# Optimization experiments

Measured on AMD Instinct MI355X. Metric: run time of the kernel, lower is better.

Reference implementation:

```python
import jax, jax.numpy as jnp
import numpy as np

N = 16384
E = 524288
IN_DIM = 128
LATENT = 48
EPS = 1e-5


def setup_inputs() -> dict:
    key = jax.random.key(0)
    ks = jax.random.split(key, 20)
    def rn(k, shape, scale=0.05):
        return jax.random.normal(k, shape, dtype=jnp.float32) * scale
    return {
        "x": jax.random.normal(ks[0], (N, IN_DIM), dtype=jnp.float32),
        "edge_index": jax.random.randint(ks[1], (2, E), 0, N, dtype=jnp.int64),
        "W1": rn(ks[2], (IN_DIM, 256)), "b1": jnp.zeros((256,), jnp.float32),
        "W2": rn(ks[3], (256, 128)),    "b2": jnp.zeros((128,), jnp.float32),
        "W3": rn(ks[4], (128, LATENT)), "b3": jnp.zeros((LATENT,), jnp.float32),
        "skip_W": rn(ks[5], (IN_DIM, LATENT)), "skip_b": jnp.zeros((LATENT,), jnp.float32),
        "bn_gamma": jnp.ones((256,), jnp.float32), "bn_beta": jnp.zeros((256,), jnp.float32),
        "bn_mean": rn(ks[6], (256,), 0.01), "bn_var": jnp.ones((256,), jnp.float32),
        "dpW1": rn(ks[7], (LATENT, 64)), "dpb1": jnp.zeros((64,), jnp.float32),
        "dpW2": rn(ks[8], (64, 1)),      "dpb2": jnp.zeros((1,), jnp.float32),
    }


def _gcn_norm(edge_index, n):
    # add self-loops, compute symmetric normalization (PyG gcn_norm)
    loops = jnp.arange(n, dtype=edge_index.dtype)
    src = jnp.concatenate([edge_index[0], loops])
    dst = jnp.concatenate([edge_index[1], loops])
    deg = jax.ops.segment_sum(jnp.ones_like(dst, dtype=jnp.float32), dst, num_segments=n)
    dinv = jnp.where(deg > 0, jax.lax.rsqrt(jnp.maximum(deg, 1.0)), 0.0)
    norm = dinv[src] * dinv[dst]  # [E+N]
    return src, dst, norm


def _gcn_conv(x, src, dst, norm, W, b, n):
    h = x @ W                                    # [N, out]
    msg = h[src] * norm[:, None]                 # gather + scale, [E+N, out]
    return jax.ops.segment_sum(msg, dst, num_segments=n) + b


def reference(x, edge_index, W1, b1, W2, b2, W3, b3, skip_W, skip_b,
              bn_gamma, bn_beta, bn_mean, bn_var, dpW1, dpb1, dpW2, dpb2):
    n = x.shape[0]
    src, dst, norm = _gcn_norm(edge_index, n)
    identity = x @ skip_W + skip_b
    h = _gcn_conv(x, src, dst, norm, W1, b1, n)
    # BatchNorm1d (inference mode: running stats), then ReLU; dropout = identity (eval)
    h = (h - bn_mean) * jax.lax.rsqrt(bn_var + EPS) * bn_gamma + bn_beta
    h = jax.nn.relu(h)
    h = jax.nn.relu(_gcn_conv(h, src, dst, norm, W2, b2, n))
    z = _gcn_conv(h, src, dst, norm, W3, b3, n) + identity   # [N, latent]
    adj_recon = jax.nn.sigmoid(z @ z.T)                      # [N, N]
    degree_pred = (jax.nn.relu(z @ dpW1 + dpb1) @ dpW2 + dpb2).squeeze(-1)
    return z, adj_recon, degree_pred
```

## Files before the change

### kernel.cpp

```cpp
#include <hip/hip_runtime.h>
#include <hip/hip_bf16.h>
#include <math.h>

#define NN   16384
#define EE   524288
#define TOTE (EE + NN)

typedef short s16x8 __attribute__((ext_vector_type(8)));
typedef float f32x16 __attribute__((ext_vector_type(16)));

__device__ inline unsigned short bf16r(float f) {
    unsigned int u = __float_as_uint(f);
    return (unsigned short)((u + 0x7FFFu + ((u >> 16) & 1u)) >> 16);
}

__global__ void k_prep(const float* __restrict__ x,  const float* __restrict__ W1,
                       const float* __restrict__ W2, const float* __restrict__ W3,
                       const float* __restrict__ skW,
                       unsigned short* __restrict__ xb,  unsigned short* __restrict__ W1t,
                       unsigned short* __restrict__ W2t, unsigned short* __restrict__ W3t,
                       unsigned short* __restrict__ skWt,
                       int* __restrict__ deg, int* __restrict__ cur) {
    const int S0 = NN * 128;
    const int S1 = S0 + 256 * 128;
    const int S2 = S1 + 128 * 256;
    const int S3 = S2 + 64 * 128;
    const int S4 = S3 + 64 * 128;
    int i = blockIdx.x * 256 + threadIdx.x;
    if (i < NN) { deg[i] = 0; cur[i] = 0; }
    if (i < S0) { xb[i] = bf16r(x[i]); }
    else if (i < S1) { int j = i - S0; int n = j >> 7, k = j & 127; W1t[j] = bf16r(W1[k * 256 + n]); }
    else if (i < S2) { int j = i - S1; int n = j >> 8, k = j & 255; W2t[j] = bf16r(W2[k * 128 + n]); }
    else if (i < S3) { int j = i - S2; int n = j >> 7, k = j & 127; W3t[j] = (n < 48) ? bf16r(W3[k * 48 + n]) : 0; }
    else if (i < S4) { int j = i - S3; int n = j >> 7, k = j & 127; skWt[j] = (n < 48) ? bf16r(skW[k * 48 + n]) : 0; }
}

__global__ void k_deg(const int* __restrict__ ei, int* __restrict__ deg) {
    int e = blockIdx.x * blockDim.x + threadIdx.x;
    if (e < EE) atomicAdd(&deg[ei[EE + e]], 1);
}

__global__ __launch_bounds__(1024) void k_scan(const int* __restrict__ deg,
                                               int* __restrict__ off,
                                               float* __restrict__ dinv) {
    __shared__ int part[1024];
    int t = threadIdx.x;
    int base = t * 16;
    int loc[16];
    int s = 0;
#pragma unroll
    for (int q = 0; q < 16; q++) {
        loc[q] = deg[base + q] + 1;
        dinv[base + q] = rsqrtf((float)loc[q]);
        s += loc[q];
    }
    part[t] = s;
    __syncthreads();
    for (int d = 1; d < 1024; d <<= 1) {
        int v = (t >= d) ? part[t - d] : 0;
        __syncthreads();
        part[t] += v;
        __syncthreads();
    }
    int ex = (t == 0) ? 0 : part[t - 1];
#pragma unroll
    for (int q = 0; q < 16; q++) { off[base + q] = ex; ex += loc[q]; }
    if (t == 1023) off[NN] = ex;
}

__global__ void k_fill(const int* __restrict__ ei, const int* __restrict__ off,
                       int* __restrict__ cur, const float* __restrict__ dinv,
                       int* __restrict__ cs, float* __restrict__ cw) {
    int e = blockIdx.x * blockDim.x + threadIdx.x;
    if (e >= TOTE) return;
    int s, d;
    if (e < EE) { s = ei[e]; d = ei[EE + e]; }
    else        { s = d = e - EE; }
    int pos = off[d] + atomicAdd(&cur[d], 1);
    cs[pos] = s;
    cw[pos] = dinv[s] * dinv[d];
}

__global__ void k_bnfold(const float* __restrict__ b1, const float* __restrict__ gamma,
                         const float* __restrict__ beta, const float* __restrict__ mean,
                         const float* __restrict__ var,
                         float* __restrict__ A, float* __restrict__ C) {
    int j = threadIdx.x;
    float a = gamma[j] * rsqrtf(var[j] + 1e-5f);
    A[j] = a;
    C[j] = (b1[j] - mean[j]) * a + beta[j];
}

template <int MODE>
__global__ void k_agg128(const unsigned short* __restrict__ H, const int* __restrict__ off,
                         const int* __restrict__ cs, const float* __restrict__ cw,
                         const float* __restrict__ bias, unsigned short* __restrict__ Y) {
    int node = blockIdx.x * 4 + (threadIdx.x >> 6);
    int lane = threadIdx.x & 63;
    int s0 = off[node], cnt = off[node + 1] - s0;
    const unsigned int* Hp = (const unsigned int*)H;
    float ax = 0.f, ay = 0.f;
    for (int base = 0; base < cnt; base += 64) {
        int nb = cnt - base; if (nb > 64) nb = 64;
        int vi = 0; float vw = 0.f;
        if (lane < nb) { vi = cs[s0 + base + lane]; vw = cw[s0 + base + lane]; }
        int e = 0;
        for (; e + 4 <= nb; e += 4) {
            int   i0 = __shfl(vi, e + 0), i1 = __shfl(vi, e + 1);
            int   i2 = __shfl(vi, e + 2), i3 = __shfl(vi, e + 3);
            float w0 = __shfl(vw, e + 0), w1 = __shfl(vw, e + 1);
            float w2 = __shfl(vw, e + 2), w3 = __shfl(vw, e + 3);
            unsigned int u0 = Hp[(size_t)i0 * 64 + lane];
            unsigned int u1 = Hp[(size_t)i1 * 64 + lane];
            unsigned int u2 = Hp[(size_t)i2 * 64 + lane];
            unsigned int u3 = Hp[(size_t)i3 * 64 + lane];
            ax += __uint_as_float(u0 << 16) * w0 + __uint_as_float(u1 << 16) * w1
                + __uint_as_float(u2 << 16) * w2 + __uint_as_float(u3 << 16) * w3;
            ay += __uint_as_float(u0 & 0xffff0000u) * w0 + __uint_as_float(u1 & 0xffff0000u) * w1
                + __uint_as_float(u2 & 0xffff0000u) * w2 + __uint_as_float(u3 & 0xffff0000u) * w3;
        }
        for (; e < nb; e++) {
            int i0 = __shfl(vi, e); float w0 = __shfl(vw, e);
            unsigned int u0 = Hp[(size_t)i0 * 64 + lane];
            ax += __uint_as_float(u0 << 16) * w0;
            ay += __uint_as_float(u0 & 0xffff0000u) * w0;
        }
    }
    if constexpr (MODE == 2) {
        ax = fmaxf(ax + bias[2 * lane], 0.f);
        ay = fmaxf(ay + bias[2 * lane + 1], 0.f);
    }
    unsigned int o = ((unsigned int)bf16r(ay) << 16) | bf16r(ax);
    ((unsigned int*)Y)[(size_t)node * 64 + lane] = o;
}

__global__ void k_aggz(const float* __restrict__ H, const int* __restrict__ off,
                       const int* __restrict__ cs, const float* __restrict__ cw,
                       const float* __restrict__ b3, const float* __restrict__ idb,
                       const float* __restrict__ dpW1, const float* __restrict__ dpb1,
                       const float* __restrict__ dpW2, const float* __restrict__ dpb2,
                       float* __restrict__ zout, unsigned short* __restrict__ zb,
                       float* __restrict__ dpout) {
    int node = blockIdx.x * 4 + (threadIdx.x >> 6);
    int lane = threadIdx.x & 63;
    int s0 = off[node], cnt = off[node + 1] - s0;
    float a = 0.f;
    for (int base = 0; base < cnt; base += 64) {
        int nb = cnt - base; if (nb > 64) nb = 64;
        int vi = 0; float vw = 0.f;
        if (lane < nb) { vi = cs[s0 + base + lane]; vw = cw[s0 + base + lane]; }
        int e = 0;
        for (; e + 4 <= nb; e += 4) {
            int   i0 = __shfl(vi, e + 0), i1 = __shfl(vi, e + 1);
            int   i2 = __shfl(vi, e + 2), i3 = __shfl(vi, e + 3);
            float w0 = __shfl(vw, e + 0), w1 = __shfl(vw, e + 1);
            float w2 = __shfl(vw, e + 2), w3 = __shfl(vw, e + 3);
            if (lane < 48) {
                float v0 = H[(size_t)i0 * 64 + lane];
                float v1 = H[(size_t)i1 * 64 + lane];
                float v2 = H[(size_t)i2 * 64 + lane];
                float v3 = H[(size_t)i3 * 64 + lane];
                a += v0 * w0 + v1 * w1 + v2 * w2 + v3 * w3;
            }
        }
        for (; e < nb; e++) {
            int i0 = __shfl(vi, e); float w0 = __shfl(vw, e);
            if (lane < 48) a += H[(size_t)i0 * 64 + lane] * w0;
        }
    }
    float zv = 0.f;
    if (lane < 48) {
        zv = a + b3[lane] + idb[(size_t)node * 64 + lane];
        zout[(size_t)node * 48 + lane] = zv;
        zb[(size_t)node * 48 + lane] = bf16r(zv);
    }
    float hj = dpb1[lane];
#pragma unroll
    for (int k = 0; k < 48; k++) hj += __shfl(zv, k) * dpW1[k * 64 + lane];
    hj = fmaxf(hj, 0.f);
    float p = hj * dpW2[lane];
    for (int o = 32; o > 0; o >>= 1) p += __shfl_down(p, o);
    if (lane == 0) dpout[node] = p + dpb2[0];
}

template <int K, int NP, int MODE, int TW>
__global__ void k_mm(const unsigned short* __restrict__ A,
                     const unsigned short* __restrict__ Bt,
                     const float* __restrict__ P0, const float* __restrict__ P1,
                     void* __restrict__ Yv) {
    int wv = threadIdx.x >> 6, l = threadIdx.x & 63;
    int ti = blockIdx.x;
    int tj = blockIdx.y * TW + wv;
    int r = l & 31, hi = l >> 5;
    const s16x8* ap = (const s16x8*)(A + (size_t)(ti * 32 + r) * K + 8 * hi);
    const s16x8* bp = (const s16x8*)(Bt + (size_t)(tj * 32 + r) * K + 8 * hi);
    f32x16 c = {};
#pragma unroll
    for (int kk = 0; kk < K / 16; kk++)
        c = __builtin_amdgcn_mfma_f32_32x32x16_bf16(ap[2 * kk], bp[2 * kk], c, 0, 0, 0);
    int col = tj * 32 + r;
#pragma unroll
    for (int reg = 0; reg < 16; reg++) {
        int row = ti * 32 + (reg & 3) + 8 * (reg >> 2) + 4 * hi;
        float v = c[reg];
        if constexpr (MODE == 1) {
            v = fmaxf(v * P0[col] + P1[col], 0.f);
            ((unsigned short*)Yv)[(size_t)row * NP + col] = bf16r(v);
        } else if constexpr (MODE == 0) {
            ((unsigned short*)Yv)[(size_t)row * NP + col] = bf16r(v);
        } else if constexpr (MODE == 2) {
            ((float*)Yv)[(size_t)row * NP + col] = v + P0[col];
        } else {
            ((float*)Yv)[(size_t)row * NP + col] = v;
        }
    }
}

__global__ __launch_bounds__(256) void k_adj2(const unsigned short* __restrict__ zb,
                                              float* __restrict__ out) {
    int wv = threadIdx.x >> 6;
    int l  = threadIdx.x & 63;
    int ti = blockIdx.y;
    int tj = blockIdx.x * 4 + wv;
    int r  = l & 31;
    int hi = l >> 5;

    const s16x8* ap = (const s16x8*)(zb + (size_t)(ti * 32 + r) * 48 + 8 * hi);
    const s16x8* bp = (const s16x8*)(zb + (size_t)(tj * 32 + r) * 48 + 8 * hi);

    f32x16 c = {};
#pragma unroll
    for (int kk = 0; kk < 3; kk++) {
        s16x8 a = ap[2 * kk];
        s16x8 b = bp[2 * kk];
        c = __builtin_amdgcn_mfma_f32_32x32x16_bf16(a, b, c, 0, 0, 0);
    }

    size_t colbase = (size_t)tj * 32 + r;
#pragma unroll
    for (int reg = 0; reg < 16; reg++) {
        int row = ti * 32 + (reg & 3) + 8 * (reg >> 2) + 4 * hi;
        float v = 1.f / (1.f + __expf(-c[reg]));
        __builtin_nontemporal_store(v, out + (size_t)row * NN + colbase);
    }
}

extern "C" void kernel_launch(void* const* d_in, const int* in_sizes, int n_in,
                              void* d_out, int out_size, void* d_ws, size_t ws_size,
                              hipStream_t stream) {
    const float* x      = (const float*)d_in[0];
    const int*   ei     = (const int*)d_in[1];
    const float* W1     = (const float*)d_in[2];
    const float* b1     = (const float*)d_in[3];
    const float* W2     = (const float*)d_in[4];
    const float* b2     = (const float*)d_in[5];
    const float* W3     = (const float*)d_in[6];
    const float* b3     = (const float*)d_in[7];
    const float* skW    = (const float*)d_in[8];
    const float* skb    = (const float*)d_in[9];
    const float* gamma  = (const float*)d_in[10];
    const float* beta   = (const float*)d_in[11];
    const float* mean   = (const float*)d_in[12];
    const float* var    = (const float*)d_in[13];
    const float* dpW1   = (const float*)d_in[14];
    const float* dpb1   = (const float*)d_in[15];
    const float* dpW2   = (const float*)d_in[16];
    const float* dpb2   = (const float*)d_in[17];

    float* zout   = (float*)d_out;
    float* adjout = zout + (size_t)NN * 48;
    float* dpout  = adjout + (size_t)NN * NN;

    char* w = (char*)d_ws;
    auto alloc = [&](size_t bytes) {
        char* p = w; w += ((bytes + 255) & ~(size_t)255); return p;
    };
    int*   deg  = (int*)alloc((size_t)NN * 4);
    int*   cur  = (int*)alloc((size_t)NN * 4);
    int*   off  = (int*)alloc((size_t)(NN + 1) * 4);
    int*   cs   = (int*)alloc((size_t)TOTE * 4);
    float* cw   = (float*)alloc((size_t)TOTE * 4);
    float* dinv = (float*)alloc((size_t)NN * 4);
    float* bnA  = (float*)alloc(256 * 4);
    float* bnC  = (float*)alloc(256 * 4);
    unsigned short* xb   = (unsigned short*)alloc((size_t)NN * 128 * 2);
    unsigned short* W1t  = (unsigned short*)alloc(256 * 128 * 2);
    unsigned short* W2t  = (unsigned short*)alloc(128 * 256 * 2);
    unsigned short* W3t  = (unsigned short*)alloc(64 * 128 * 2);
    unsigned short* skWt = (unsigned short*)alloc(64 * 128 * 2);
    unsigned short* xa   = (unsigned short*)alloc((size_t)NN * 128 * 2);
    unsigned short* h1   = (unsigned short*)alloc((size_t)NN * 256 * 2);
    unsigned short* h2   = (unsigned short*)alloc((size_t)NN * 128 * 2);
    unsigned short* h2a  = (unsigned short*)alloc((size_t)NN * 128 * 2);
    float* h3   = (float*)alloc((size_t)NN * 64 * 4);
    float* idb  = (float*)alloc((size_t)NN * 64 * 4);
    unsigned short* zb = (unsigned short*)alloc((size_t)NN * 48 * 2);

    const int PREP = NN * 128 + 256 * 128 + 128 * 256 + 64 * 128 + 64 * 128;
    k_prep<<<(PREP + 255) / 256, 256, 0, stream>>>(x, W1, W2, W3, skW,
                                                   xb, W1t, W2t, W3t, skWt, deg, cur);
    k_deg<<<EE / 256, 256, 0, stream>>>(ei, deg);
    k_scan<<<1, 1024, 0, stream>>>(deg, off, dinv);
    k_fill<<<TOTE / 256, 256, 0, stream>>>(ei, off, cur, dinv, cs, cw);
    k_bnfold<<<1, 256, 0, stream>>>(b1, gamma, beta, mean, var, bnA, bnC);

    k_agg128<0><<<NN / 4, 256, 0, stream>>>(xb, off, cs, cw, nullptr, xa);
    k_mm<128, 256, 1, 4><<<dim3(NN / 32, 2), 256, 0, stream>>>(xa, W1t, bnA, bnC, h1);
    k_mm<256, 128, 0, 4><<<dim3(NN / 32, 1), 256, 0, stream>>>(h1, W2t, nullptr, nullptr, h2);
    k_agg128<2><<<NN / 4, 256, 0, stream>>>(h2, off, cs, cw, b2, h2a);
    k_mm<128, 64, 3, 2><<<dim3(NN / 32, 1), 128, 0, stream>>>(h2a, W3t, nullptr, nullptr, h3);
    k_mm<128, 64, 2, 2><<<dim3(NN / 32, 1), 128, 0, stream>>>(xb, skWt, skb, nullptr, idb);
    k_aggz<<<NN / 4, 256, 0, stream>>>(h3, off, cs, cw, b3, idb,
                                       dpW1, dpb1, dpW2, dpb2, zout, zb, dpout);

    k_adj2<<<dim3(128, 512), 256, 0, stream>>>(zb, adjout);
}
```

Measured before the change: 329.8 us.

## Merge small kernels and unroll aggregation gathers by eight

Folds the batch-norm parameter computation into the prep kernel and merges the two small W3 and skip matmuls into a single launch indexed by blockIdx.y, cutting two kernel launches. The gather loops in both aggregation kernels are unrolled from four to eight edges, issuing all loads before the FMAs to raise memory-level parallelism. This adds register pressure. The adjacency output kernel, which is likely the dominant cost, is unchanged.

```diff
diff --git a/kernel.cpp b/kernel.cpp
--- a/kernel.cpp
+++ b/kernel.cpp
@@ -17,9 +17,13 @@
 __global__ void k_prep(const float* __restrict__ x,  const float* __restrict__ W1,
                        const float* __restrict__ W2, const float* __restrict__ W3,
                        const float* __restrict__ skW,
+                       const float* __restrict__ b1, const float* __restrict__ gamma,
+                       const float* __restrict__ beta, const float* __restrict__ mean,
+                       const float* __restrict__ var,
                        unsigned short* __restrict__ xb,  unsigned short* __restrict__ W1t,
                        unsigned short* __restrict__ W2t, unsigned short* __restrict__ W3t,
                        unsigned short* __restrict__ skWt,
+                       float* __restrict__ bnA, float* __restrict__ bnC,
                        int* __restrict__ deg, int* __restrict__ cur) {
     const int S0 = NN * 128;
     const int S1 = S0 + 256 * 128;
@@ -33,6 +37,12 @@
     else if (i < S2) { int j = i - S1; int n = j >> 8, k = j & 255; W2t[j] = bf16r(W2[k * 128 + n]); }
     else if (i < S3) { int j = i - S2; int n = j >> 7, k = j & 127; W3t[j] = (n < 48) ? bf16r(W3[k * 48 + n]) : 0; }
     else if (i < S4) { int j = i - S3; int n = j >> 7, k = j & 127; skWt[j] = (n < 48) ? bf16r(skW[k * 48 + n]) : 0; }
+    else if (i < S4 + 256) {
+        int j = i - S4;
+        float a = gamma[j] * rsqrtf(var[j] + 1e-5f);
+        bnA[j] = a;
+        bnC[j] = (b1[j] - mean[j]) * a + beta[j];
+    }
 }
 
 __global__ void k_deg(const int* __restrict__ ei, int* __restrict__ deg) {
@@ -79,16 +89,6 @@
     int pos = off[d] + atomicAdd(&cur[d], 1);
     cs[pos] = s;
     cw[pos] = dinv[s] * dinv[d];
-}
-
-__global__ void k_bnfold(const float* __restrict__ b1, const float* __restrict__ gamma,
-                         const float* __restrict__ beta, const float* __restrict__ mean,
-                         const float* __restrict__ var,
-                         float* __restrict__ A, float* __restrict__ C) {
-    int j = threadIdx.x;
-    float a = gamma[j] * rsqrtf(var[j] + 1e-5f);
-    A[j] = a;
-    C[j] = (b1[j] - mean[j]) * a + beta[j];
 }
 
 template <int MODE>
@@ -105,19 +105,19 @@
         int vi = 0; float vw = 0.f;
         if (lane < nb) { vi = cs[s0 + base + lane]; vw = cw[s0 + base + lane]; }
         int e = 0;
-        for (; e + 4 <= nb; e += 4) {
-            int   i0 = __shfl(vi, e + 0), i1 = __shfl(vi, e + 1);
-            int   i2 = __shfl(vi, e + 2), i3 = __shfl(vi, e + 3);
-            float w0 = __shfl(vw, e + 0), w1 = __shfl(vw, e + 1);
-            float w2 = __shfl(vw, e + 2), w3 = __shfl(vw, e + 3);
-            unsigned int u0 = Hp[(size_t)i0 * 64 + lane];
-            unsigned int u1 = Hp[(size_t)i1 * 64 + lane];
-            unsigned int u2 = Hp[(size_t)i2 * 64 + lane];
-            unsigned int u3 = Hp[(size_t)i3 * 64 + lane];
-            ax += __uint_as_float(u0 << 16) * w0 + __uint_as_float(u1 << 16) * w1
-                + __uint_as_float(u2 << 16) * w2 + __uint_as_float(u3 << 16) * w3;
-            ay += __uint_as_float(u0 & 0xffff0000u) * w0 + __uint_as_float(u1 & 0xffff0000u) * w1
-                + __uint_as_float(u2 & 0xffff0000u) * w2 + __uint_as_float(u3 & 0xffff0000u) * w3;
+        for (; e + 8 <= nb; e += 8) {
+            unsigned int u[8]; float ww[8];
+#pragma unroll
+            for (int q = 0; q < 8; q++) {
+                int   iq = __shfl(vi, e + q);
+                ww[q]    = __shfl(vw, e + q);
+                u[q] = Hp[(size_t)iq * 64 + lane];
+            }
+#pragma unroll
+            for (int q = 0; q < 8; q++) {
+                ax += __uint_as_float(u[q] << 16) * ww[q];
+                ay += __uint_as_float(u[q] & 0xffff0000u) * ww[q];
+            }
         }
         for (; e < nb; e++) {
             int i0 = __shfl(vi, e); float w0 = __shfl(vw, e);
@@ -150,18 +150,16 @@
         int vi = 0; float vw = 0.f;
         if (lane < nb) { vi = cs[s0 + base + lane]; vw = cw[s0 + base + lane]; }
         int e = 0;
-        for (; e + 4 <= nb; e += 4) {
-            int   i0 = __shfl(vi, e + 0), i1 = __shfl(vi, e + 1);
-            int   i2 = __shfl(vi, e + 2), i3 = __shfl(vi, e + 3);
-            float w0 = __shfl(vw, e + 0), w1 = __shfl(vw, e + 1);
-            float w2 = __shfl(vw, e + 2), w3 = __shfl(vw, e + 3);
-            if (lane < 48) {
-                float v0 = H[(size_t)i0 * 64 + lane];
-                float v1 = H[(size_t)i1 * 64 + lane];
-                float v2 = H[(size_t)i2 * 64 + lane];
-                float v3 = H[(size_t)i3 * 64 + lane];
-                a += v0 * w0 + v1 * w1 + v2 * w2 + v3 * w3;
+        for (; e + 8 <= nb; e += 8) {
+            float v[8], ww[8];
+#pragma unroll
+            for (int q = 0; q < 8; q++) {
+                int   iq = __shfl(vi, e + q);
+                ww[q]    = __shfl(vw, e + q);
+                v[q] = (lane < 48) ? H[(size_t)iq * 64 + lane] : 0.f;
             }
+#pragma unroll
+            for (int q = 0; q < 8; q++) a += v[q] * ww[q];
         }
         for (; e < nb; e++) {
             int i0 = __shfl(vi, e); float w0 = __shfl(vw, e);
@@ -213,6 +211,34 @@
         } else {
             ((float*)Yv)[(size_t)row * NP + col] = v;
         }
+    }
+}
+
+__global__ void k_mm3s(const unsigned short* __restrict__ h2a,
+                       const unsigned short* __restrict__ W3t,
+                       const unsigned short* __restrict__ xb,
+                       const unsigned short* __restrict__ skWt,
+                       const float* __restrict__ skb,
+                       float* __restrict__ h3, float* __restrict__ idb) {
+    int wv = threadIdx.x >> 6, l = threadIdx.x & 63;
+    int ti = blockIdx.x;
+    int tj = wv;
+    int r = l & 31, hi = l >> 5;
+    const unsigned short* A  = (blockIdx.y == 0) ? h2a : xb;
+    const unsigned short* Bt = (blockIdx.y == 0) ? W3t : skWt;
+    const s16x8* ap = (const s16x8*)(A + (size_t)(ti * 32 + r) * 128 + 8 * hi);
+    const s16x8* bp = (const s16x8*)(Bt + (size_t)(tj * 32 + r) * 128 + 8 * hi);
+    f32x16 c = {};
+#pragma unroll
+    for (int kk = 0; kk < 8; kk++)
+        c = __builtin_amdgcn_mfma_f32_32x32x16_bf16(ap[2 * kk], bp[2 * kk], c, 0, 0, 0);
+    int col = tj * 32 + r;
+    float add = (blockIdx.y == 0) ? 0.f : ((col < 48) ? skb[col] : 0.f);
+    float* Y = (blockIdx.y == 0) ? h3 : idb;
+#pragma unroll
+    for (int reg = 0; reg < 16; reg++) {
+        int row = ti * 32 + (reg & 3) + 8 * (reg >> 2) + 4 * hi;
+        Y[(size_t)row * 64 + col] = c[reg] + add;
     }
 }
 
@@ -296,20 +322,20 @@
     float* idb  = (float*)alloc((size_t)NN * 64 * 4);
     unsigned short* zb = (unsigned short*)alloc((size_t)NN * 48 * 2);
 
-    const int PREP = NN * 128 + 256 * 128 + 128 * 256 + 64 * 128 + 64 * 128;
+    const int PREP = NN * 128 + 256 * 128 + 128 * 256 + 64 * 128 + 64 * 128 + 256;
     k_prep<<<(PREP + 255) / 256, 256, 0, stream>>>(x, W1, W2, W3, skW,
-                                                   xb, W1t, W2t, W3t, skWt, deg, cur);
+                                                   b1, gamma, beta, mean, var,
+                                                   xb, W1t, W2t, W3t, skWt,
+                                                   bnA, bnC, deg, cur);
     k_deg<<<EE / 256, 256, 0, stream>>>(ei, deg);
     k_scan<<<1, 1024, 0, stream>>>(deg, off, dinv);
     k_fill<<<TOTE / 256, 256, 0, stream>>>(ei, off, cur, dinv, cs, cw);
-    k_bnfold<<<1, 256, 0, stream>>>(b1, gamma, beta, mean, var, bnA, bnC);
 
     k_agg128<0><<<NN / 4, 256, 0, stream>>>(xb, off, cs, cw, nullptr, xa);
     k_mm<128, 256, 1, 4><<<dim3(NN / 32, 2), 256, 0, stream>>>(xa, W1t, bnA, bnC, h1);
     k_mm<256, 128, 0, 4><<<dim3(NN / 32, 1), 256, 0, stream>>>(h1, W2t, nullptr, nullptr, h2);
     k_agg128<2><<<NN / 4, 256, 0, stream>>>(h2, off, cs, cw, b2, h2a);
-    k_mm<128, 64, 3, 2><<<dim3(NN / 32, 1), 128, 0, stream>>>(h2a, W3t, nullptr, nullptr, h3);
-    k_mm<128, 64, 2, 2><<<dim3(NN / 32, 1), 128, 0, stream>>>(xb, skWt, skb, nullptr, idb);
+    k_mm3s<<<dim3(NN / 32, 2), 128, 0, stream>>>(h2a, W3t, xb, skWt, skb, h3, idb);
     k_aggz<<<NN / 4, 256, 0, stream>>>(h3, off, cs, cw, b3, idb,
                                        dpW1, dpb1, dpW2, dpb2, zout, zb, dpout);
 
```

Result: no change. 324.7 us (-1.5%).
